# Kernel optimization log

Measured on AMD Instinct MI355X. Metric: run time of the kernel, lower is better.

The kernel has to match this reference:

```python
import jax, jax.numpy as jnp
import numpy as np

D_MODEL = 1024
NUM_HEADS = 16
HEAD_DIM = D_MODEL // NUM_HEADS
B, S = 2, 2048


def setup_inputs() -> dict:
    key = jax.random.key(0)
    ks = jax.random.split(key, 6)
    scale = 0.02
    return {
        "x": jax.random.normal(ks[0], (B, S, D_MODEL), dtype=jnp.float32),
        "mask": jax.random.normal(ks[1], (S, S), dtype=jnp.float32),
        "Wqkv": jax.random.normal(ks[2], (D_MODEL, 3 * D_MODEL), dtype=jnp.float32) * scale,
        "bqkv": jax.random.normal(ks[3], (3 * D_MODEL,), dtype=jnp.float32) * scale,
        "Wout": jax.random.normal(ks[4], (D_MODEL, D_MODEL), dtype=jnp.float32) * scale,
        "bout": jax.random.normal(ks[5], (D_MODEL,), dtype=jnp.float32) * scale,
    }


def reference(x, mask, Wqkv, bqkv, Wout, bout):
    b, s, d = x.shape
    h, hd = NUM_HEADS, HEAD_DIM
    qkv = x @ Wqkv + bqkv                              # [b, s, 3d]
    qkv = qkv.reshape(b, s, h, 3 * hd).transpose(0, 2, 1, 3)  # [b, h, s, 3hd]
    q, k, v = jnp.split(qkv, 3, axis=-1)               # each [b, h, s, hd]
    scaled = jnp.einsum("bhqd,bhkd->bhqk", q, k) / jnp.sqrt(jnp.float32(hd))
    scaled = scaled + mask                             # mask [s, s] broadcasts
    attn = jax.nn.softmax(scaled, axis=-1)
    values = jnp.einsum("bhqk,bhkd->bhqd", attn, v)    # [b, h, s, hd]
    values = values.transpose(0, 2, 1, 3).reshape(b, s, d)
    return values @ Wout + bout
```

## Files before the change

kernel.cpp:

```cpp
#include <hip/hip_runtime.h>
#include <hip/hip_bf16.h>

#define D_MODEL 1024
#define NH 16
#define HD 64
#define BATCH 2
#define SEQ 2048
#define M_TOTAL (BATCH*SEQ)

typedef _Float16 f16;
typedef _Float16 half8 __attribute__((ext_vector_type(8)));
typedef _Float16 half4v __attribute__((ext_vector_type(4)));
typedef float floatx4 __attribute__((ext_vector_type(4)));

#if __has_builtin(__builtin_amdgcn_exp2f)
#define EXP2(x) __builtin_amdgcn_exp2f(x)
#else
#define EXP2(x) __expf(0.6931471805599453f * (x))
#endif

__device__ inline void gload_lds16(const void* g, void* l) {
    __builtin_amdgcn_global_load_lds(
        (const __attribute__((address_space(1))) unsigned int*)g,
        (__attribute__((address_space(3))) unsigned int*)l, 16, 0, 0);
}

__global__ void cvt_f32_f16(const float* __restrict__ src, f16* __restrict__ dst, int n4) {
    int i = blockIdx.x * blockDim.x + threadIdx.x;
    if (i < n4) {
        float4 v = ((const float4*)src)[i];
        half4v o = { (f16)v.x, (f16)v.y, (f16)v.z, (f16)v.w };
        *(half4v*)(dst + (long)i * 4) = o;
    }
}

__global__ void l2scale_cvt(const float* __restrict__ src, f16* __restrict__ dst, int n4) {
    int i = blockIdx.x * blockDim.x + threadIdx.x;
    if (i < n4) {
        float4 v = ((const float4*)src)[i];
        const float L2E = 1.44269504f;
        half4v o = { (f16)(v.x * L2E), (f16)(v.y * L2E), (f16)(v.z * L2E), (f16)(v.w * L2E) };
        *(half4v*)(dst + (long)i * 4) = o;
    }
}

__global__ void transpose_cvt(const float* __restrict__ src, f16* __restrict__ dst, int R, int C) {
    __shared__ float tile[32][33];
    int tx = threadIdx.x;
    int ty = threadIdx.y;
    int c0 = blockIdx.x * 32;
    int r0 = blockIdx.y * 32;
    for (int yy = 0; yy < 32; yy += 8)
        tile[ty + yy][tx] = src[(long)(r0 + ty + yy) * C + c0 + tx];
    __syncthreads();
    for (int yy = 0; yy < 32; yy += 8)
        dst[(long)(c0 + ty + yy) * R + r0 + tx] = (f16)tile[tx][ty + yy];
}

template<int MODE, int TN>
__global__ __launch_bounds__(256) void gemm_mfma(
    const f16* __restrict__ A, const f16* __restrict__ BT,
    const float* __restrict__ bias,
    f16* __restrict__ Qh, f16* __restrict__ Kh, f16* __restrict__ Vtg,
    float* __restrict__ out, int Kdim)
{
    constexpr int NF = TN / 32;
    __shared__ f16 Ah[128 * 64];
    __shared__ f16 Bh[TN * 64];
    int tid  = threadIdx.x;
    int wid  = tid >> 6;
    int lane = tid & 63;
    int quad = lane >> 4;
    int l16  = lane & 15;

    int id  = blockIdx.y * gridDim.x + blockIdx.x;
    int xcd = id & 7;
    int s   = id >> 3;
    constexpr int CN = (MODE == 0) ? 12 : 8;
    int n0 = ((xcd & 1) * CN + s % CN) * TN;
    int m0 = ((xcd >> 1) * 8 + s / CN) * 128;

    int mrow = (wid >> 1) * 64;
    int ncol = (wid & 1) * (TN / 2);
    int grow = lane >> 3;
    int gchunk = (lane & 7) ^ (grow & 7);
    int sw0 = ((quad)     ^ (l16 & 7)) * 8;
    int sw1 = ((quad + 4) ^ (l16 & 7)) * 8;

    floatx4 acc[4][NF];
    #pragma unroll
    for (int mb = 0; mb < 4; mb++)
        #pragma unroll
        for (int nb = 0; nb < NF; nb++) acc[mb][nb] = (floatx4){0.f, 0.f, 0.f, 0.f};

    const f16* Abase = A + (long)m0 * Kdim;
    const f16* Bbase = BT + (long)n0 * Kdim;

    for (int k0 = 0; k0 < Kdim; k0 += 64) {
        #pragma unroll
        for (int j = 0; j < 4; j++) {
            int r = j * 32 + wid * 8 + grow;
            gload_lds16(Abase + (long)r * Kdim + k0 + gchunk * 8, &Ah[(j * 32 + wid * 8) * 64]);
        }
        #pragma unroll
        for (int j = 0; j < TN / 32; j++) {
            int r = j * 32 + wid * 8 + grow;
            gload_lds16(Bbase + (long)r * Kdim + k0 + gchunk * 8, &Bh[(j * 32 + wid * 8) * 64]);
        }
        __syncthreads();
        #pragma unroll
        for (int h = 0; h < 2; h++) {
            int sw = h ? sw1 : sw0;
            half8 af[4];
            #pragma unroll
            for (int mb = 0; mb < 4; mb++)
                af[mb] = *(const half8*)&Ah[(mrow + mb * 16 + l16) * 64 + sw];
            #pragma unroll
            for (int nb = 0; nb < NF; nb++) {
                half8 bf = *(const half8*)&Bh[(ncol + nb * 16 + l16) * 64 + sw];
                #pragma unroll
                for (int mb = 0; mb < 4; mb++)
                    acc[mb][nb] = __builtin_amdgcn_mfma_f32_16x16x32_f16(af[mb], bf, acc[mb][nb], 0, 0, 0);
            }
        }
        __syncthreads();
    }

    #pragma unroll
    for (int nb = 0; nb < NF; nb++) {
        int n = n0 + ncol + nb * 16 + l16;
        float bv = bias[n];
        int head = 0, t = 0, d = 0;
        if (MODE == 0) { head = n / 192; int rem = n % 192; t = rem / 64; d = rem % 64; }
        #pragma unroll
        for (int mb = 0; mb < 4; mb++) {
            int mbase = m0 + mrow + mb * 16 + quad * 4;
            if (MODE == 0) {
                int b = mbase >> 11;
                int ss = mbase & 2047;
                long bh = b * NH + head;
                if (t == 2) {
                    half4v pack;
                    #pragma unroll
                    for (int r = 0; r < 4; r++) pack[r] = (f16)(acc[mb][nb][r] + bv);
                    *(half4v*)&Vtg[(bh * HD + d) * SEQ + ss] = pack;
                } else if (t == 0) {
                    #pragma unroll
                    for (int r = 0; r < 4; r++)
                        Qh[(bh * SEQ + ss + r) * HD + d] = (f16)((acc[mb][nb][r] + bv) * 0.18033688f);
                } else {
                    #pragma unroll
                    for (int r = 0; r < 4; r++)
                        Kh[(bh * SEQ + ss + r) * HD + d] = (f16)(acc[mb][nb][r] + bv);
                }
            } else {
                #pragma unroll
                for (int r = 0; r < 4; r++)
                    out[(long)(mbase + r) * D_MODEL + n] = acc[mb][nb][r] + bv;
            }
        }
    }
}

__global__ __launch_bounds__(256) void attn(
    const f16* __restrict__ Qh, const f16* __restrict__ Kh, const f16* __restrict__ Vtg,
    const f16* __restrict__ E, f16* __restrict__ valh)
{
    __shared__ f16 Kl[2][64 * 64];
    __shared__ f16 Vt[2][64 * 64];
    __shared__ f16 Pl[4][32 * 68];
    int tid  = threadIdx.x;
    int wid  = tid >> 6;
    int lane = tid & 63;
    int quad = lane >> 4;
    int l16  = lane & 15;

    int id   = blockIdx.y * 16 + blockIdx.x;
    int xcd  = id & 7;
    int slot = id >> 3;
    int bh   = ((xcd & 3) << 3) | (slot >> 3);
    int qx   = ((xcd >> 2) << 3) | (slot & 7);
    int b  = bh >> 4;
    int h  = bh & 15;
    int qblk = qx * 128;
    int q0 = qblk + wid * 32;

    int grow = lane >> 3;
    int gchunk = (lane & 7) ^ (grow & 7);
    int sw0 = ((quad)     ^ (l16 & 7)) * 8;
    int sw1 = ((quad + 4) ^ (l16 & 7)) * 8;

    const f16* Qbase = Qh + ((long)bh * SEQ + q0) * HD;
    half8 qf[2][2];
    #pragma unroll
    for (int m = 0; m < 2; m++)
        #pragma unroll
        for (int c = 0; c < 2; c++)
            qf[m][c] = *(const half8*)&Qbase[(long)(m * 16 + l16) * HD + c * 32 + quad * 8];

    half8 onesv;
    #pragma unroll
    for (int j = 0; j < 8; j++) onesv[j] = (f16)1.0f;

    floatx4 Of[2][4];
    floatx4 ssum[2];
    #pragma unroll
    for (int m = 0; m < 2; m++) {
        ssum[m] = (floatx4){0.f, 0.f, 0.f, 0.f};
        #pragma unroll
        for (int nb = 0; nb < 4; nb++) Of[m][nb] = (floatx4){0.f, 0.f, 0.f, 0.f};
    }

    const f16* Kb = Kh + (long)bh * SEQ * HD;
    const f16* Vb = Vtg + (long)bh * HD * SEQ;
    const f16* Eb = E + (long)qblk * SEQ;

    auto stage = [&](int buf, int k0) {
        #pragma unroll
        for (int j = 0; j < 2; j++) {
            int r = j * 32 + wid * 8 + grow;
            gload_lds16(Kb + (long)(k0 + r) * HD + gchunk * 8, &Kl[buf][(j * 32 + wid * 8) * 64]);
            gload_lds16(Vb + (long)r * SEQ + k0 + gchunk * 8, &Vt[buf][(j * 32 + wid * 8) * 64]);
        }
    };

    stage(0, 0);
    __syncthreads();

    auto iter = [&](const int buf, int k0) {
        bool notlast = (k0 + 64 < SEQ);
        if (notlast) stage(buf ^ 1, k0 + 64);

        f16 ef[2][4][4];
        #pragma unroll
        for (int m = 0; m < 2; m++)
            #pragma unroll
            for (int r = 0; r < 4; r++) {
                const f16* Erow = Eb + (long)(wid * 32 + m * 16 + quad * 4 + r) * SEQ + k0 + l16;
                #pragma unroll
                for (int kb = 0; kb < 4; kb++) ef[m][r][kb] = Erow[kb * 16];
            }

        floatx4 sc[2][4];
        __builtin_amdgcn_s_setprio(1);
        #pragma unroll
        for (int kb = 0; kb < 4; kb++) {
            half8 kf0 = *(const half8*)&Kl[buf][(kb * 16 + l16) * 64 + sw0];
            half8 kf1 = *(const half8*)&Kl[buf][(kb * 16 + l16) * 64 + sw1];
            #pragma unroll
            for (int m = 0; m < 2; m++) {
                floatx4 sacc = (floatx4){0.f, 0.f, 0.f, 0.f};
                sacc = __builtin_amdgcn_mfma_f32_16x16x32_f16(qf[m][0], kf0, sacc, 0, 0, 0);
                sacc = __builtin_amdgcn_mfma_f32_16x16x32_f16(qf[m][1], kf1, sacc, 0, 0, 0);
                sc[m][kb] = sacc;
            }
        }
        __builtin_amdgcn_s_setprio(0);

        #pragma unroll
        for (int m = 0; m < 2; m++)
            #pragma unroll
            for (int kb = 0; kb < 4; kb++)
                #pragma unroll
                for (int r = 0; r < 4; r++) {
                    float p = EXP2(sc[m][kb][r] + (float)ef[m][r][kb]);
                    Pl[wid][(m * 16 + quad * 4 + r) * 68 + kb * 16 + l16] = (f16)p;
                }

        half8 pf[2][2];
        #pragma unroll
        for (int m = 0; m < 2; m++)
            #pragma unroll
            for (int c = 0; c < 2; c++)
                pf[m][c] = *(const half8*)&Pl[wid][(m * 16 + l16) * 68 + c * 32 + quad * 8];

        __builtin_amdgcn_s_setprio(1);
        #pragma unroll
        for (int m = 0; m < 2; m++) {
            ssum[m] = __builtin_amdgcn_mfma_f32_16x16x32_f16(pf[m][0], onesv, ssum[m], 0, 0, 0);
            ssum[m] = __builtin_amdgcn_mfma_f32_16x16x32_f16(pf[m][1], onesv, ssum[m], 0, 0, 0);
        }
        #pragma unroll
        for (int nb = 0; nb < 4; nb++) {
            half8 vf0 = *(const half8*)&Vt[buf][(nb * 16 + l16) * 64 + sw0];
            half8 vf1 = *(const half8*)&Vt[buf][(nb * 16 + l16) * 64 + sw1];
            #pragma unroll
            for (int m = 0; m < 2; m++) {
                Of[m][nb] = __builtin_amdgcn_mfma_f32_16x16x32_f16(pf[m][0], vf0, Of[m][nb], 0, 0, 0);
                Of[m][nb] = __builtin_amdgcn_mfma_f32_16x16x32_f16(pf[m][1], vf1, Of[m][nb], 0, 0, 0);
            }
        }
        __builtin_amdgcn_s_setprio(0);

        __syncthreads();
    };

    for (int k0 = 0; k0 < SEQ; k0 += 128) {
        iter(0, k0);
        iter(1, k0 + 64);
    }

    float rinv[2][4];
    #pragma unroll
    for (int m = 0; m < 2; m++)
        #pragma unroll
        for (int r = 0; r < 4; r++) rinv[m][r] = 1.f / ssum[m][r];

    #pragma unroll
    for (int m = 0; m < 2; m++)
        #pragma unroll
        for (int nb = 0; nb < 4; nb++)
            #pragma unroll
            for (int r = 0; r < 4; r++) {
                int q = q0 + m * 16 + quad * 4 + r;
                int d = nb * 16 + l16;
                valh[((long)(b * SEQ + q)) * D_MODEL + h * HD + d] = (f16)(Of[m][nb][r] * rinv[m][r]);
            }
}

extern "C" void kernel_launch(void* const* d_in, const int* in_sizes, int n_in,
                              void* d_out, int out_size, void* d_ws, size_t ws_size,
                              hipStream_t stream) {
    const float* x    = (const float*)d_in[0];
    const float* mask = (const float*)d_in[1];
    const float* Wqkv = (const float*)d_in[2];
    const float* bqkv = (const float*)d_in[3];
    const float* Wout = (const float*)d_in[4];
    const float* bout = (const float*)d_in[5];
    float* out = (float*)d_out;

    char* ws = (char*)d_ws;
    f16* xh    = (f16*)(ws + 0);
    f16* E     = (f16*)(ws + 0);
    f16* WqkvT = (f16*)(ws + 8388608);
    f16* WoutT = (f16*)(ws + 14680064);
    f16* Qh    = (f16*)(ws + 16777216);
    f16* Kh    = (f16*)(ws + 25165824);
    f16* Vtg   = (f16*)(ws + 33554432);
    f16* valh  = (f16*)(ws + 41943040);

    cvt_f32_f16<<<4096, 256, 0, stream>>>(x, xh, M_TOTAL * D_MODEL / 4);
    transpose_cvt<<<dim3(96, 32), dim3(32, 8), 0, stream>>>(Wqkv, WqkvT, 1024, 3072);
    transpose_cvt<<<dim3(32, 32), dim3(32, 8), 0, stream>>>(Wout, WoutT, 1024, 1024);
    gemm_mfma<0, 128><<<dim3(24, 32), 256, 0, stream>>>(xh, WqkvT, bqkv, Qh, Kh, Vtg, nullptr, 1024);
    l2scale_cvt<<<4096, 256, 0, stream>>>(mask, E, SEQ * SEQ / 4);
    attn<<<dim3(16, 32), 256, 0, stream>>>(Qh, Kh, Vtg, E, valh);
    gemm_mfma<1, 64><<<dim3(16, 32), 256, 0, stream>>>(valh, WoutT, bout, nullptr, nullptr, nullptr, out, 1024);
}
```

Measured before the change: 222.8 us.

## Split attention key range across two warp groups per block with LDS reduction

The attention kernel now runs 8 waves per block: four query groups times two key groups, each key group handling alternating 64-key tiles. Both tiles are loaded together each step with a sync before compute, which drops the previous double-buffered prefetch overlap. Partial O and row sums are reduced through LDS at the end. The aim is more waves in flight per CU to hide latency, at the cost of extra barriers and lost load/compute overlap.

Result: slower. 318.2 us (+42.8%).

```diff
diff --git a/kernel.cpp b/kernel.cpp
--- a/kernel.cpp
+++ b/kernel.cpp
@@ -162,18 +162,23 @@
     }
 }
 
-__global__ __launch_bounds__(256) void attn(
+__global__ __launch_bounds__(512, 4) void attn(
     const f16* __restrict__ Qh, const f16* __restrict__ Kh, const f16* __restrict__ Vtg,
     const f16* __restrict__ E, f16* __restrict__ valh)
 {
-    __shared__ f16 Kl[2][64 * 64];
-    __shared__ f16 Vt[2][64 * 64];
-    __shared__ f16 Pl[4][32 * 68];
+    extern __shared__ f16 sm[];
+    f16* Kt0 = sm;
+    f16* Kt1 = sm + 4096;
+    f16* Vt0 = sm + 8192;
+    f16* Vt1 = sm + 12288;
+    f16* Plb = sm + 16384;
     int tid  = threadIdx.x;
     int wid  = tid >> 6;
     int lane = tid & 63;
     int quad = lane >> 4;
     int l16  = lane & 15;
+    int qg = wid & 3;
+    int kg = wid >> 2;
 
     int id   = blockIdx.y * 16 + blockIdx.x;
     int xcd  = id & 7;
@@ -183,7 +188,7 @@
     int b  = bh >> 4;
     int h  = bh & 15;
     int qblk = qx * 128;
-    int q0 = qblk + wid * 32;
+    int q0 = qblk + qg * 32;
 
     int grow = lane >> 3;
     int gchunk = (lane & 7) ^ (grow & 7);
@@ -215,28 +220,37 @@
     const f16* Vb = Vtg + (long)bh * HD * SEQ;
     const f16* Eb = E + (long)qblk * SEQ;
 
-    auto stage = [&](int buf, int k0) {
-        #pragma unroll
-        for (int j = 0; j < 2; j++) {
-            int r = j * 32 + wid * 8 + grow;
-            gload_lds16(Kb + (long)(k0 + r) * HD + gchunk * 8, &Kl[buf][(j * 32 + wid * 8) * 64]);
-            gload_lds16(Vb + (long)r * SEQ + k0 + gchunk * 8, &Vt[buf][(j * 32 + wid * 8) * 64]);
-        }
-    };
-
-    stage(0, 0);
-    __syncthreads();
-
-    auto iter = [&](const int buf, int k0) {
-        bool notlast = (k0 + 64 < SEQ);
-        if (notlast) stage(buf ^ 1, k0 + 64);
+    int stile = wid >> 1;
+    f16* sdst = (stile == 0) ? Kt0 : (stile == 1) ? Kt1 : (stile == 2) ? Vt0 : Vt1;
+    bool sK = (stile < 2);
+    int skodd = stile & 1;
+
+    f16* Kt = kg ? Kt1 : Kt0;
+    f16* Vt = kg ? Vt1 : Vt0;
+    f16* Pl = Plb + wid * (32 * 68);
+
+    for (int t = 0; t < 16; ++t) {
+        if (t) __syncthreads();
+        {
+            int kk = (2 * t + skodd) * 64;
+            #pragma unroll
+            for (int j = 0; j < 4; j++) {
+                int r = (wid & 1) * 32 + j * 8 + grow;
+                const f16* src = sK ? (Kb + (long)(kk + r) * HD + gchunk * 8)
+                                    : (Vb + (long)r * SEQ + kk + gchunk * 8);
+                gload_lds16(src, &sdst[((wid & 1) * 32 + j * 8) * 64]);
+            }
+        }
+        __syncthreads();
+
+        int k0 = (2 * t + kg) * 64;
 
         f16 ef[2][4][4];
         #pragma unroll
         for (int m = 0; m < 2; m++)
             #pragma unroll
             for (int r = 0; r < 4; r++) {
-                const f16* Erow = Eb + (long)(wid * 32 + m * 16 + quad * 4 + r) * SEQ + k0 + l16;
+                const f16* Erow = Eb + (long)(qg * 32 + m * 16 + quad * 4 + r) * SEQ + k0 + l16;
                 #pragma unroll
                 for (int kb = 0; kb < 4; kb++) ef[m][r][kb] = Erow[kb * 16];
             }
@@ -245,8 +259,8 @@
         __builtin_amdgcn_s_setprio(1);
         #pragma unroll
         for (int kb = 0; kb < 4; kb++) {
-            half8 kf0 = *(const half8*)&Kl[buf][(kb * 16 + l16) * 64 + sw0];
-            half8 kf1 = *(const half8*)&Kl[buf][(kb * 16 + l16) * 64 + sw1];
+            half8 kf0 = *(const half8*)&Kt[(kb * 16 + l16) * 64 + sw0];
+            half8 kf1 = *(const half8*)&Kt[(kb * 16 + l16) * 64 + sw1];
             #pragma unroll
             for (int m = 0; m < 2; m++) {
                 floatx4 sacc = (floatx4){0.f, 0.f, 0.f, 0.f};
@@ -264,7 +278,7 @@
                 #pragma unroll
                 for (int r = 0; r < 4; r++) {
                     float p = EXP2(sc[m][kb][r] + (float)ef[m][r][kb]);
-                    Pl[wid][(m * 16 + quad * 4 + r) * 68 + kb * 16 + l16] = (f16)p;
+                    Pl[(m * 16 + quad * 4 + r) * 68 + kb * 16 + l16] = (f16)p;
                 }
 
         half8 pf[2][2];
@@ -272,7 +286,7 @@
         for (int m = 0; m < 2; m++)
             #pragma unroll
             for (int c = 0; c < 2; c++)
-                pf[m][c] = *(const half8*)&Pl[wid][(m * 16 + l16) * 68 + c * 32 + quad * 8];
+                pf[m][c] = *(const half8*)&Pl[(m * 16 + l16) * 68 + c * 32 + quad * 8];
 
         __builtin_amdgcn_s_setprio(1);
         #pragma unroll
@@ -282,8 +296,8 @@
         }
         #pragma unroll
         for (int nb = 0; nb < 4; nb++) {
-            half8 vf0 = *(const half8*)&Vt[buf][(nb * 16 + l16) * 64 + sw0];
-            half8 vf1 = *(const half8*)&Vt[buf][(nb * 16 + l16) * 64 + sw1];
+            half8 vf0 = *(const half8*)&Vt[(nb * 16 + l16) * 64 + sw0];
+            half8 vf1 = *(const half8*)&Vt[(nb * 16 + l16) * 64 + sw1];
             #pragma unroll
             for (int m = 0; m < 2; m++) {
                 Of[m][nb] = __builtin_amdgcn_mfma_f32_16x16x32_f16(pf[m][0], vf0, Of[m][nb], 0, 0, 0);
@@ -291,31 +305,46 @@
             }
         }
         __builtin_amdgcn_s_setprio(0);
-
-        __syncthreads();
-    };
-
-    for (int k0 = 0; k0 < SEQ; k0 += 128) {
-        iter(0, k0);
-        iter(1, k0 + 64);
-    }
-
-    float rinv[2][4];
-    #pragma unroll
-    for (int m = 0; m < 2; m++)
-        #pragma unroll
-        for (int r = 0; r < 4; r++) rinv[m][r] = 1.f / ssum[m][r];
-
-    #pragma unroll
-    for (int m = 0; m < 2; m++)
-        #pragma unroll
-        for (int nb = 0; nb < 4; nb++)
-            #pragma unroll
-            for (int r = 0; r < 4; r++) {
-                int q = q0 + m * 16 + quad * 4 + r;
-                int d = nb * 16 + l16;
-                valh[((long)(b * SEQ + q)) * D_MODEL + h * HD + d] = (f16)(Of[m][nb][r] * rinv[m][r]);
-            }
+    }
+
+    __syncthreads();
+    float* xch = (float*)sm;
+    float* p = xch + (long)(qg * 64 + lane) * 48;
+    if (kg == 1) {
+        #pragma unroll
+        for (int m = 0; m < 2; m++)
+            #pragma unroll
+            for (int nb = 0; nb < 4; nb++)
+                *(floatx4*)(p + (m * 4 + nb) * 4) = Of[m][nb];
+        *(floatx4*)(p + 32) = ssum[0];
+        *(floatx4*)(p + 40) = ssum[1];
+    }
+    __syncthreads();
+    if (kg == 0) {
+        #pragma unroll
+        for (int m = 0; m < 2; m++) {
+            #pragma unroll
+            for (int nb = 0; nb < 4; nb++)
+                Of[m][nb] += *(const floatx4*)(p + (m * 4 + nb) * 4);
+            ssum[m] += *(const floatx4*)(p + 32 + m * 8);
+        }
+        float rinv[2][4];
+        #pragma unroll
+        for (int m = 0; m < 2; m++)
+            #pragma unroll
+            for (int r = 0; r < 4; r++) rinv[m][r] = 1.f / ssum[m][r];
+
+        #pragma unroll
+        for (int m = 0; m < 2; m++)
+            #pragma unroll
+            for (int nb = 0; nb < 4; nb++)
+                #pragma unroll
+                for (int r = 0; r < 4; r++) {
+                    int q = q0 + m * 16 + quad * 4 + r;
+                    int d = nb * 16 + l16;
+                    valh[((long)(b * SEQ + q)) * D_MODEL + h * HD + d] = (f16)(Of[m][nb][r] * rinv[m][r]);
+                }
+    }
 }
 
 extern "C" void kernel_launch(void* const* d_in, const int* in_sizes, int n_in,
@@ -344,6 +373,6 @@
     transpose_cvt<<<dim3(32, 32), dim3(32, 8), 0, stream>>>(Wout, WoutT, 1024, 1024);
     gemm_mfma<0, 128><<<dim3(24, 32), 256, 0, stream>>>(xh, WqkvT, bqkv, Qh, Kh, Vtg, nullptr, 1024);
     l2scale_cvt<<<4096, 256, 0, stream>>>(mask, E, SEQ * SEQ / 4);
-    attn<<<dim3(16, 32), 256, 0, stream>>>(Qh, Kh, Vtg, E, valh);
+    attn<<<dim3(16, 32), 512, 67584, stream>>>(Qh, Kh, Vtg, E, valh);
     gemm_mfma<1, 64><<<dim3(16, 32), 256, 0, stream>>>(valh, WoutT, bout, nullptr, nullptr, nullptr, out, 1024);
 }
```
